# Performance work log

Measured on AMD Instinct MI355X. Metric: run time of the kernel, lower is better.

Reference implementation:

```python
import jax, jax.numpy as jnp
import numpy as np

N = 100000   # nodes
E = 1600000  # edges (avg degree 16)
F = 64       # conv_out_dim (= in_channels here)
EDGE_DIM = 16
B = 64       # graphs in batch
DEG = np.array([0, 1000, 2000, 4000, 8000, 16000, 24000, 20000, 12000, 6000, 3000, 2000, 1000, 500, 300, 200, 100], dtype=np.float64)
AVG_LOG = float((np.log(np.arange(len(DEG)) + 1.0) * DEG).sum() / DEG.sum())  # avg_deg['log']

def setup_inputs() -> dict:
    key = jax.random.key(0)
    ks = jax.random.split(key, 16)
    def w(k, shape, fan_in):
        return (jax.random.normal(k, shape, jnp.float32) / np.sqrt(fan_in)).astype(jnp.float32)
    return {
        "x": jax.random.normal(ks[0], (N, F), jnp.float32),
        "edge_attr": jax.random.normal(ks[1], (E, EDGE_DIM), jnp.float32),
        "edge_index": jax.random.randint(ks[2], (2, E), 0, N, jnp.int32),
        "batch": jnp.sort(jax.random.randint(ks[3], (N,), 0, B, jnp.int32)),
        # pre_mlp: Linear(F, F//2) -> ReLU -> Linear(F//2, F)
        "W1": w(ks[4], (F, F // 2), F), "b1": jnp.zeros((F // 2,), jnp.float32),
        "W2": w(ks[5], (F // 2, F), F // 2), "b2": jnp.zeros((F,), jnp.float32),
        # CEALConv (PNA-style) params
        "We": w(ks[6], (EDGE_DIM, F), EDGE_DIM), "be": jnp.zeros((F,), jnp.float32),   # edge encoder
        "Wp": w(ks[7], (3 * F, F), 3 * F), "bp": jnp.zeros((F,), jnp.float32),          # pre_nn
        "Wo": w(ks[8], (13 * F, F), 13 * F), "bo": jnp.zeros((F,), jnp.float32),        # post_nn ((4 agg * 3 scalers + 1) * F)
        "Wl": w(ks[9], (F, F), F), "bl": jnp.zeros((F,), jnp.float32),                  # final lin
        # BatchNorm affine
        "gamma": jnp.ones((F,), jnp.float32), "beta": jnp.zeros((F,), jnp.float32),
        # post_mlp: Linear(F, 100) -> ReLU -> Linear(100, 1)
        "Wm1": w(ks[10], (F, 100), F), "bm1": jnp.zeros((100,), jnp.float32),
        "Wm2": w(ks[11], (100, 1), 100), "bm2": jnp.zeros((1,), jnp.float32),
    }

def reference(x, edge_attr, edge_index, batch, W1, b1, W2, b2, We, be, Wp, bp, Wo, bo, Wl, bl, gamma, beta, Wm1, bm1, Wm2, bm2):
    src, dst = edge_index[0], edge_index[1]
    # pre-MLP on node features
    x = jax.nn.relu(x @ W1 + b1) @ W2 + b2                                  # [N, F]
    # message: pre_nn(cat[x_i, x_j, edge_encoder(edge_attr)]) -- split Wp to avoid concat
    e = edge_attr @ We + be                                                 # [E, F]
    h = x[dst] @ Wp[:F] + x[src] @ Wp[F:2 * F] + e @ Wp[2 * F:] + bp        # [E, F]
    # multi-aggregator scatter (mean, min, max, std) at destination nodes
    cnt = jax.ops.segment_sum(jnp.ones((E,), h.dtype), dst, N)              # in-degree [N]
    d = jnp.maximum(cnt, 1.0)[:, None]
    mean = jax.ops.segment_sum(h, dst, N) / d
    mean2 = jax.ops.segment_sum(h * h, dst, N) / d
    std = jnp.sqrt(jax.nn.relu(mean2 - mean * mean) + 1e-5)
    has = (cnt > 0)[:, None]
    mn = jnp.where(has, jax.ops.segment_min(h, dst, N), 0.0)
    mx = jnp.where(has, jax.ops.segment_max(h, dst, N), 0.0)
    agg = jnp.concatenate([mean, mn, mx, std], axis=-1)                     # [N, 4F]
    # degree scalers: identity, amplification, attenuation
    amp = jnp.log(d + 1.0) / AVG_LOG
    scaled = jnp.concatenate([agg, agg * amp, agg / amp], axis=-1)          # [N, 12F]
    # post_nn(cat[x, scaled]) then final linear
    out = jnp.concatenate([x, scaled], axis=-1) @ Wo + bo                   # [N, F]
    out = out @ Wl + bl
    # BatchNorm (batch statistics) + ReLU
    mu = out.mean(axis=0)
    var = out.var(axis=0)
    out = (out - mu) * jax.lax.rsqrt(var + 1e-5) * gamma + beta
    out = jax.nn.relu(out)
    # global_add_pool over graphs, then post-MLP head
    pooled = jax.ops.segment_sum(out, batch, B)                             # [B, F]
    return jax.nn.relu(pooled @ Wm1 + bm1) @ Wm2 + bm2                      # [B, 1]
```

## Files before the change

### kernel.cpp

```cpp
#include <hip/hip_runtime.h>
#include <hip/hip_bf16.h>
#include <math.h>

#define NN 100000
#define NE 1600000
#define FF 64
#define NB 64
#define NSCAN_BLOCKS 391

__device__ __constant__ float AVG_LOG_F = 1.9595436f;

typedef short short8 __attribute__((ext_vector_type(8)));
typedef float f32x4 __attribute__((ext_vector_type(4)));

__device__ __forceinline__ void atomAddF(float* p, float v) {
    __hip_atomic_fetch_add(p, v, __ATOMIC_RELAXED, __HIP_MEMORY_SCOPE_AGENT);
}
__device__ __forceinline__ float bf2f(short v) {
    return __uint_as_float(((unsigned)(unsigned short)v) << 16);
}
__device__ __forceinline__ unsigned packbf2(float a, float b) {
    unsigned ua = (unsigned)(unsigned short)__bfloat16_as_short(__float2bfloat16(a));
    unsigned ub = (unsigned)(unsigned short)__bfloat16_as_short(__float2bfloat16(b));
    return ua | (ub << 16);
}
__device__ __forceinline__ unsigned lds_pair(const unsigned short* p) {
    unsigned u;
    __builtin_memcpy(&u, p, 4);
    return u;
}
__device__ __forceinline__ float dot2bf(unsigned a, unsigned b, float c) {
    float d;
    asm("v_dot2_f32_bf16 %0, %1, %2, %3" : "=v"(d) : "v"(a), "v"(b), "v"(c));
    return d;
}

__global__ void fold_weights(const float* __restrict__ Wo, const float* __restrict__ Wl,
                             const float* __restrict__ bo, const float* __restrict__ bl,
                             const float* __restrict__ We, const float* __restrict__ Wp,
                             const float* __restrict__ bp, const float* __restrict__ be,
                             __hip_bfloat16* __restrict__ Wtb,
                             unsigned* __restrict__ Wepp,
                             float* __restrict__ bpF, float* __restrict__ boF) {
    int t = blockIdx.x * blockDim.x + threadIdx.x;
    if (t < 832 * 64) {
        int k = t >> 6, f = t & 63;
        float acc = 0.f;
        for (int j = 0; j < 64; j++) acc += Wo[k * 64 + j] * Wl[j * 64 + f];
        Wtb[f * 832 + k] = __float2bfloat16(acc);
    } else if (t < 832 * 64 + 512) {
        int u = t - 832 * 64; int k2 = u >> 6, f = u & 63;
        float a0 = 0.f, a1 = 0.f;
        for (int j = 0; j < 64; j++) {
            float wp = Wp[(128 + j) * 64 + f];
            a0 += We[(2 * k2) * 64 + j] * wp;
            a1 += We[(2 * k2 + 1) * 64 + j] * wp;
        }
        Wepp[k2 * 64 + f] = packbf2(a0, a1);
    } else if (t < 832 * 64 + 512 + 64) {
        int f = t - (832 * 64 + 512);
        float acc = bl[f];
        for (int j = 0; j < 64; j++) acc += bo[j] * Wl[j * 64 + f];
        boF[f] = acc;
    } else if (t < 832 * 64 + 512 + 128) {
        int f = t - (832 * 64 + 512 + 64);
        float acc = bp[f];
        for (int j = 0; j < 64; j++) acc += be[j] * Wp[(128 + j) * 64 + f];
        bpF[f] = acc;
    }
}

__global__ __launch_bounds__(256) void node_pre(const float* __restrict__ x,
                                                const float* __restrict__ W1, const float* __restrict__ b1,
                                                const float* __restrict__ W2, const float* __restrict__ b2,
                                                const float* __restrict__ Wp,
                                                float* __restrict__ x2, float* __restrict__ A,
                                                __hip_bfloat16* __restrict__ Bnb) {
    __shared__ unsigned short xs[4][64], ts[4][32], x2s[4][64];
    int tid = threadIdx.x;
    int w = tid >> 6, f = tid & 63;
    int fm = f & 31;

    unsigned w1p[32], w2p[16], wp0p[32], wp1p[32];
    #pragma unroll
    for (int k2 = 0; k2 < 32; ++k2)
        w1p[k2] = packbf2(W1[(2 * k2) * 32 + fm], W1[(2 * k2 + 1) * 32 + fm]);
    #pragma unroll
    for (int k2 = 0; k2 < 16; ++k2)
        w2p[k2] = packbf2(W2[(2 * k2) * 64 + f], W2[(2 * k2 + 1) * 64 + f]);
    #pragma unroll
    for (int k2 = 0; k2 < 32; ++k2) {
        wp0p[k2] = packbf2(Wp[(2 * k2) * 64 + f], Wp[(2 * k2 + 1) * 64 + f]);
        wp1p[k2] = packbf2(Wp[4096 + (2 * k2) * 64 + f], Wp[4096 + (2 * k2 + 1) * 64 + f]);
    }
    float b1f = b1[fm], b2f = b2[f];

    int wid = blockIdx.x * 4 + w;
    int nw = gridDim.x * 4;
    for (int v = wid; v < NN; v += nw) {
        float xv = x[(size_t)v * 64 + f];
        xs[w][f] = (unsigned short)__bfloat16_as_short(__float2bfloat16(xv));
        float t = b1f;
        #pragma unroll
        for (int k2 = 0; k2 < 32; ++k2) t = dot2bf(lds_pair(&xs[w][2 * k2]), w1p[k2], t);
        t = fmaxf(t, 0.f);
        if (f < 32) ts[w][f] = (unsigned short)__bfloat16_as_short(__float2bfloat16(t));
        float acc2 = b2f;
        #pragma unroll
        for (int k2 = 0; k2 < 16; ++k2) acc2 = dot2bf(lds_pair(&ts[w][2 * k2]), w2p[k2], acc2);
        x2[(size_t)v * 64 + f] = acc2;
        x2s[w][f] = (unsigned short)__bfloat16_as_short(__float2bfloat16(acc2));
        float aa = 0.f, bb = 0.f;
        #pragma unroll
        for (int k2 = 0; k2 < 32; ++k2) {
            unsigned xq = lds_pair(&x2s[w][2 * k2]);
            aa = dot2bf(xq, wp0p[k2], aa);
            bb = dot2bf(xq, wp1p[k2], bb);
        }
        A[(size_t)v * 64 + f] = aa;
        Bnb[(size_t)v * 64 + f] = __float2bfloat16(bb);
    }
}

__global__ void hist_kernel(const int* __restrict__ ei, unsigned* __restrict__ cnt_i) {
    int t = blockIdx.x * blockDim.x + threadIdx.x;
    if (t < NE) atomicAdd(&cnt_i[ei[NE + t]], 1u);
}

__global__ void scan_blocksum(const unsigned* __restrict__ cnt_i, unsigned* __restrict__ bsum) {
    __shared__ unsigned red[256];
    int t = blockIdx.x * 256 + threadIdx.x;
    unsigned c = (t < NN) ? cnt_i[t] : 0u;
    red[threadIdx.x] = c; __syncthreads();
    for (int s = 128; s > 0; s >>= 1) {
        if (threadIdx.x < s) red[threadIdx.x] += red[threadIdx.x + s];
        __syncthreads();
    }
    if (threadIdx.x == 0) bsum[blockIdx.x] = red[0];
}

__global__ void scan_top(const unsigned* __restrict__ bsum, unsigned* __restrict__ boff,
                         unsigned* __restrict__ start) {
    __shared__ unsigned sh[512];
    int t = threadIdx.x;
    unsigned v = (t < NSCAN_BLOCKS) ? bsum[t] : 0u;
    sh[t] = v; __syncthreads();
    for (int d = 1; d < 512; d <<= 1) {
        unsigned add = (t >= d) ? sh[t - d] : 0u;
        __syncthreads();
        sh[t] += add;
        __syncthreads();
    }
    if (t < NSCAN_BLOCKS) boff[t] = sh[t] - v;
    if (t == 0) start[NN] = NE;
}

__global__ void scan_final(const unsigned* __restrict__ cnt_i, const unsigned* __restrict__ boff,
                           unsigned* __restrict__ start) {
    __shared__ unsigned sh[256];
    int b = blockIdx.x, t = threadIdx.x;
    int v = b * 256 + t;
    unsigned c = (v < NN) ? cnt_i[v] : 0u;
    sh[t] = c; __syncthreads();
    for (int d = 1; d < 256; d <<= 1) {
        unsigned add = (t >= d) ? sh[t - d] : 0u;
        __syncthreads();
        sh[t] += add;
        __syncthreads();
    }
    if (v < NN) start[v] = boff[b] + sh[t] - c;
}

__global__ void scatter_kernel(const int* __restrict__ ei, const float* __restrict__ ea,
                               const unsigned* __restrict__ start,
                               unsigned* __restrict__ cnt_i,
                               __hip_bfloat16* __restrict__ eab, int* __restrict__ src_s) {
    int t = blockIdx.x * blockDim.x + threadIdx.x;
    if (t == 0) {
        src_s[NE] = 0;
        short8 z = {0, 0, 0, 0, 0, 0, 0, 0};
        short8* p = (short8*)(eab + (size_t)NE * 16);
        p[0] = z; p[1] = z;
    }
    if (t < NE) {
        int d = ei[NE + t];
        unsigned old = atomicSub(&cnt_i[d], 1u);
        unsigned pos = start[d] + old - 1u;
        src_s[pos] = ei[t];
        const float4* s4 = (const float4*)(ea + (size_t)t * 16);
        float4 a = s4[0], b = s4[1], c = s4[2], e = s4[3];
        short8 o0, o1;
        o0[0] = (short)__bfloat16_as_short(__float2bfloat16(a.x));
        o0[1] = (short)__bfloat16_as_short(__float2bfloat16(a.y));
        o0[2] = (short)__bfloat16_as_short(__float2bfloat16(a.z));
        o0[3] = (short)__bfloat16_as_short(__float2bfloat16(a.w));
        o0[4] = (short)__bfloat16_as_short(__float2bfloat16(b.x));
        o0[5] = (short)__bfloat16_as_short(__float2bfloat16(b.y));
        o0[6] = (short)__bfloat16_as_short(__float2bfloat16(b.z));
        o0[7] = (short)__bfloat16_as_short(__float2bfloat16(b.w));
        o1[0] = (short)__bfloat16_as_short(__float2bfloat16(c.x));
        o1[1] = (short)__bfloat16_as_short(__float2bfloat16(c.y));
        o1[2] = (short)__bfloat16_as_short(__float2bfloat16(c.z));
        o1[3] = (short)__bfloat16_as_short(__float2bfloat16(c.w));
        o1[4] = (short)__bfloat16_as_short(__float2bfloat16(e.x));
        o1[5] = (short)__bfloat16_as_short(__float2bfloat16(e.y));
        o1[6] = (short)__bfloat16_as_short(__float2bfloat16(e.z));
        o1[7] = (short)__bfloat16_as_short(__float2bfloat16(e.w));
        short8* dst8 = (short8*)(eab + (size_t)pos * 16);
        dst8[0] = o0; dst8[1] = o1;
    }
}

__global__ __launch_bounds__(256) void deg_localhist(const unsigned* __restrict__ start,
                                                     unsigned* __restrict__ bh,
                                                     unsigned* __restrict__ rank_g) {
    __shared__ unsigned short keys[256];
    int t0 = threadIdx.x, b = blockIdx.x;
    int t = b * 256 + t0;
    unsigned d = 0xFFFFu;
    if (t < NN) {
        d = start[t + 1] - start[t];
        if (d > 255u) d = 255u;
    }
    keys[t0] = (unsigned short)d;
    __syncthreads();
    unsigned cnt = 0;
    #pragma unroll 8
    for (int i = 0; i < 256; ++i) cnt += (keys[i] == (unsigned short)t0) ? 1u : 0u;
    bh[t0 * NSCAN_BLOCKS + b] = cnt;
    if (t < NN) {
        unsigned r = 0;
        for (int i = 0; i < t0; ++i) r += (keys[i] == (unsigned short)d) ? 1u : 0u;
        rank_g[t] = r;
    }
}

__global__ __launch_bounds__(256) void deg_colscan(const unsigned* __restrict__ bh,
                                                   unsigned* __restrict__ bhoff) {
    __shared__ unsigned sh[256];
    int bin = threadIdx.x;
    unsigned s = 0;
    for (int b = 0; b < NSCAN_BLOCKS; ++b) s += bh[bin * NSCAN_BLOCKS + b];
    sh[bin] = s;
    __syncthreads();
    for (int d = 1; d < 256; d <<= 1) {
        unsigned add = (bin >= d) ? sh[bin - d] : 0u;
        __syncthreads();
        sh[bin] += add;
        __syncthreads();
    }
    unsigned run = sh[bin] - s;
    for (int b = 0; b < NSCAN_BLOCKS; ++b) {
        unsigned c = bh[bin * NSCAN_BLOCKS + b];
        bhoff[bin * NSCAN_BLOCKS + b] = run;
        run += c;
    }
}

__global__ __launch_bounds__(256) void deg_place(const unsigned* __restrict__ start,
                                                 const unsigned* __restrict__ bhoff,
                                                 const unsigned* __restrict__ rank_g,
                                                 int* __restrict__ perm) {
    int t0 = threadIdx.x, b = blockIdx.x;
    int t = b * 256 + t0;
    if (t < NN) {
        unsigned d = start[t + 1] - start[t];
        if (d > 255u) d = 255u;
        perm[bhoff[d * NSCAN_BLOCKS + b] + rank_g[t]] = t;
    }
}

__global__ __launch_bounds__(256) void agg_post_kernel(const __hip_bfloat16* __restrict__ eab,
                                                       const int* __restrict__ src_s,
                                                       const unsigned* __restrict__ start,
                                                       const int* __restrict__ perm,
                                                       const float* __restrict__ A,
                                                       const unsigned short* __restrict__ Bnb,
                                                       const float* __restrict__ x2,
                                                       const unsigned* __restrict__ Wepp, const float* __restrict__ bpF,
                                                       const __hip_bfloat16* __restrict__ Wtb,
                                                       const float* __restrict__ boF,
                                                       float* __restrict__ out_pre,
                                                       float* __restrict__ bnsum, float* __restrict__ bnsum2) {
    __shared__ __hip_bfloat16 As[16 * 840];
    __shared__ int pvs[16];
    int tid = threadIdx.x;
    int w = __builtin_amdgcn_readfirstlane(tid >> 6);
    int f = tid & 63;
    int base = blockIdx.x * 16;

    unsigned wcolp[8];
    #pragma unroll
    for (int k = 0; k < 8; k++) wcolp[k] = Wepp[k * 64 + f];
    float bpf = bpF[f];

    int vv[4]; unsigned s0[4]; int len[4], lim[4]; float av[4];
    float sA[4] = {0.f, 0.f, 0.f, 0.f}, s2A[4] = {0.f, 0.f, 0.f, 0.f};
    float mnA[4], mxA[4];
    int maxlen = 0;
    #pragma unroll
    for (int g = 0; g < 4; ++g) {
        int v = __builtin_amdgcn_readfirstlane(perm[base + g * 4 + w]);
        vv[g] = v;
        if (f == 0) pvs[g * 4 + w] = v;
        unsigned a = start[v], b = start[v + 1];
        s0[g] = a; len[g] = (int)(b - a);
        lim[g] = len[g] > 0 ? len[g] - 1 : 0;
        maxlen = max(maxlen, len[g]);
        av[g] = A[(size_t)v * 64 + f] + bpf;
        mnA[g] = INFINITY; mxA[g] = -INFINITY;
    }

    for (int j = 0; j < maxlen; ++j) {
        #pragma unroll
        for (int g = 0; g < 4; ++g) {
            unsigned idx = s0[g] + (unsigned)min(j, lim[g]);
            const unsigned* e32 = (const unsigned*)(eab + (size_t)idx * 16);
            int src = src_s[idx];
            const unsigned short* brow = Bnb + ((size_t)src << 6);
            float h = av[g];
            #pragma unroll
            for (int k = 0; k < 8; k++) h = dot2bf(e32[k], wcolp[k], h);
            h += bf2f((short)brow[f]);
            bool valid = j < len[g];
            float hm = valid ? h : 0.f;
            sA[g] += hm; s2A[g] += hm * hm;
            mnA[g] = fminf(mnA[g], h);
            mxA[g] = fmaxf(mxA[g], h);
        }
    }

    #pragma unroll
    for (int g = 0; g < 4; ++g) {
        int n = g * 4 + w;
        int v = vv[g];
        float c = (float)len[g];
        float d = fmaxf(c, 1.f);
        float inv = 1.f / d;
        float mean = sA[g] * inv, mean2 = s2A[g] * inv;
        float sd = sqrtf(fmaxf(mean2 - mean * mean, 0.f) + 1e-5f);
        bool has = len[g] > 0;
        float mn = has ? mnA[g] : 0.f;
        float mx = has ? mxA[g] : 0.f;
        float l = __logf(d + 1.f);
        float amp = l * (1.0f / 1.9595436f);
        float iamp = 1.9595436f / l;
        __hip_bfloat16* row = &As[n * 840];
        row[f]        = __float2bfloat16(x2[(size_t)v * 64 + f]);
        row[64 + f]   = __float2bfloat16(mean);
        row[128 + f]  = __float2bfloat16(mn);
        row[192 + f]  = __float2bfloat16(mx);
        row[256 + f]  = __float2bfloat16(sd);
        row[320 + f]  = __float2bfloat16(mean * amp);
        row[384 + f]  = __float2bfloat16(mn * amp);
        row[448 + f]  = __float2bfloat16(mx * amp);
        row[512 + f]  = __float2bfloat16(sd * amp);
        row[576 + f]  = __float2bfloat16(mean * iamp);
        row[640 + f]  = __float2bfloat16(mn * iamp);
        row[704 + f]  = __float2bfloat16(mx * iamp);
        row[768 + f]  = __float2bfloat16(sd * iamp);
    }
    __syncthreads();

    int m = f & 15, q = f >> 4;
    int fbase = w * 16;
    f32x4 acc = {0.f, 0.f, 0.f, 0.f};
    const __hip_bfloat16* arow = &As[m * 840 + q * 8];
    const __hip_bfloat16* brow = &Wtb[(size_t)(fbase + m) * 832 + q * 8];
    #pragma unroll
    for (int s = 0; s < 26; ++s) {
        short8 af = *(const short8*)(arow + s * 32);
        short8 bf = *(const short8*)(brow + s * 32);
        acc = __builtin_amdgcn_mfma_f32_16x16x32_bf16(af, bf, acc, 0, 0, 0);
    }

    float bof = boF[fbase + m];
    float p1 = 0.f, p2 = 0.f;
    #pragma unroll
    for (int r = 0; r < 4; ++r) {
        float vvv = acc[r] + bof;
        int vn = pvs[q * 4 + r];
        out_pre[(size_t)vn * 64 + fbase + m] = vvv;
        p1 += vvv; p2 += vvv * vvv;
    }
    p1 += __shfl_xor(p1, 16); p2 += __shfl_xor(p2, 16);
    p1 += __shfl_xor(p1, 32); p2 += __shfl_xor(p2, 32);
    if (f < 16) {
        atomAddF(&bnsum[fbase + f], p1);
        atomAddF(&bnsum2[fbase + f], p2);
    }
}

__global__ __launch_bounds__(256) void bn_pool(const float* __restrict__ out_pre, const int* __restrict__ batch,
                                               const float* __restrict__ bnsum, const float* __restrict__ bnsum2,
                                               const float* __restrict__ gamma, const float* __restrict__ beta,
                                               float* __restrict__ pooled) {
    __shared__ float red[256];
    int tid = threadIdx.x, f = tid & 63, q = tid >> 6;
    int base = blockIdx.x * 64;
    float mu = bnsum[f] * (1.0f / NN);
    float var = bnsum2[f] * (1.0f / NN) - mu * mu;
    float sc = gamma[f] * rsqrtf(var + 1e-5f);
    float sh = beta[f] - mu * sc;
    int b_first = batch[base < NN ? base : NN - 1];
    int last = base + 63; if (last >= NN) last = NN - 1;
    int b_last = batch[last];
    if (b_first == b_last) {
        float local = 0.f;
        for (int g = 0; g < 16; ++g) {
            int v = base + g * 4 + q;
            if (v < NN) local += fmaxf(out_pre[(size_t)v * 64 + f] * sc + sh, 0.f);
        }
        red[tid] = local;
        __syncthreads();
        if (tid < 64) atomAddF(&pooled[b_first * 64 + f], red[f] + red[f + 64] + red[f + 128] + red[f + 192]);
    } else {
        for (int g = 0; g < 16; ++g) {
            int v = base + g * 4 + q;
            if (v < NN) {
                float val = fmaxf(out_pre[(size_t)v * 64 + f] * sc + sh, 0.f);
                atomAddF(&pooled[batch[v] * 64 + f], val);
            }
        }
    }
}

__global__ void head_kernel(const float* __restrict__ pooled,
                            const float* __restrict__ Wm1, const float* __restrict__ bm1,
                            const float* __restrict__ Wm2, const float* __restrict__ bm2,
                            float* __restrict__ out) {
    __shared__ float ts[64][104];
    int tid = threadIdx.x;
    for (int t = tid; t < 64 * 100; t += 256) {
        int b = t / 100, j = t % 100;
        float acc = bm1[j];
        for (int k = 0; k < 64; k++) acc += pooled[b * 64 + k] * Wm1[k * 100 + j];
        ts[b][j] = fmaxf(acc, 0.f);
    }
    __syncthreads();
    if (tid < 64) {
        float acc = bm2[0];
        for (int j = 0; j < 100; j++) acc += ts[tid][j] * Wm2[j];
        out[tid] = acc;
    }
}

extern "C" void kernel_launch(void* const* d_in, const int* in_sizes, int n_in,
                              void* d_out, int out_size, void* d_ws, size_t ws_size,
                              hipStream_t stream) {
    const float* x    = (const float*)d_in[0];
    const float* ea   = (const float*)d_in[1];
    const int*   ei   = (const int*)d_in[2];
    const int*   batch= (const int*)d_in[3];
    const float* W1   = (const float*)d_in[4];
    const float* b1   = (const float*)d_in[5];
    const float* W2   = (const float*)d_in[6];
    const float* b2   = (const float*)d_in[7];
    const float* We   = (const float*)d_in[8];
    const float* be   = (const float*)d_in[9];
    const float* Wp   = (const float*)d_in[10];
    const float* bp   = (const float*)d_in[11];
    const float* Wo   = (const float*)d_in[12];
    const float* bo   = (const float*)d_in[13];
    const float* Wl   = (const float*)d_in[14];
    const float* bl   = (const float*)d_in[15];
    const float* gamma= (const float*)d_in[16];
    const float* beta = (const float*)d_in[17];
    const float* Wm1  = (const float*)d_in[18];
    const float* bm1  = (const float*)d_in[19];
    const float* Wm2  = (const float*)d_in[20];
    const float* bm2  = (const float*)d_in[21];

    float* ws = (float*)d_ws;
    constexpr size_t NF = (size_t)NN * 64;
    const size_t o_x2     = 0;
    const size_t o_B      = NF;
    const size_t o_A      = 2 * NF;
    const size_t o_outpre = 3 * NF;
    const size_t o_start  = 4 * NF;
    const size_t o_cnt_i  = o_start + 100016;
    const size_t o_bsum   = o_cnt_i + 100000;
    const size_t o_boff   = o_bsum + 512;
    const size_t o_perm   = o_boff + 512;
    const size_t o_eab    = o_perm + 100000;
    const size_t o_srcs   = o_eab + 12800016;
    const size_t o_Wtb    = o_srcs + 1600016;
    const size_t o_Wepp   = o_Wtb + 26624;
    const size_t o_bpF    = o_Wepp + 512;
    const size_t o_boF    = o_bpF + 64;
    const size_t o_bnscale= o_boF + 64;
    const size_t o_bnshift= o_bnscale + 64;
    const size_t o_pooled = o_bnshift + 64;
    const size_t o_bnsum  = o_pooled + 64 * 64;
    const size_t o_bnsum2 = o_bnsum + 64;

    unsigned* bh     = (unsigned*)(ws + o_cnt_i);
    unsigned* bhoff  = (unsigned*)(ws + o_outpre);
    unsigned* rank_g = (unsigned*)(ws + o_outpre + 100096);

    hipMemsetAsync(ws + o_cnt_i, 0, 100000 * sizeof(unsigned), stream);
    hipMemsetAsync(ws + o_pooled, 0, (64 * 64 + 128) * sizeof(float), stream);

    fold_weights<<<213, 256, 0, stream>>>(Wo, Wl, bo, bl, We, Wp, bp, be,
                                          (__hip_bfloat16*)(ws + o_Wtb), (unsigned*)(ws + o_Wepp),
                                          ws + o_bpF, ws + o_boF);
    node_pre<<<768, 256, 0, stream>>>(x, W1, b1, W2, b2, Wp,
                                      ws + o_x2, ws + o_A, (__hip_bfloat16*)(ws + o_B));
    hist_kernel<<<6250, 256, 0, stream>>>(ei, (unsigned*)(ws + o_cnt_i));
    scan_blocksum<<<NSCAN_BLOCKS, 256, 0, stream>>>((unsigned*)(ws + o_cnt_i), (unsigned*)(ws + o_bsum));
    scan_top<<<1, 512, 0, stream>>>((unsigned*)(ws + o_bsum), (unsigned*)(ws + o_boff),
                                    (unsigned*)(ws + o_start));
    scan_final<<<NSCAN_BLOCKS, 256, 0, stream>>>((unsigned*)(ws + o_cnt_i), (unsigned*)(ws + o_boff),
                                                 (unsigned*)(ws + o_start));
    scatter_kernel<<<6250, 256, 0, stream>>>(ei, ea, (const unsigned*)(ws + o_start),
                                             (unsigned*)(ws + o_cnt_i),
                                             (__hip_bfloat16*)(ws + o_eab), (int*)(ws + o_srcs));
    deg_localhist<<<NSCAN_BLOCKS, 256, 0, stream>>>((const unsigned*)(ws + o_start), bh, rank_g);
    deg_colscan<<<1, 256, 0, stream>>>(bh, bhoff);
    deg_place<<<NSCAN_BLOCKS, 256, 0, stream>>>((const unsigned*)(ws + o_start), bhoff, rank_g,
                                                (int*)(ws + o_perm));
    agg_post_kernel<<<6250, 256, 0, stream>>>((const __hip_bfloat16*)(ws + o_eab),
                                              (const int*)(ws + o_srcs),
                                              (const unsigned*)(ws + o_start),
                                              (const int*)(ws + o_perm),
                                              ws + o_A, (const unsigned short*)(ws + o_B), ws + o_x2,
                                              (const unsigned*)(ws + o_Wepp), ws + o_bpF,
                                              (const __hip_bfloat16*)(ws + o_Wtb), ws + o_boF,
                                              ws + o_outpre, ws + o_bnsum, ws + o_bnsum2);
    bn_pool<<<1563, 256, 0, stream>>>(ws + o_outpre, batch,
                                      ws + o_bnsum, ws + o_bnsum2, gamma, beta, ws + o_pooled);
    head_kernel<<<1, 256, 0, stream>>>(ws + o_pooled, Wm1, bm1, Wm2, bm2, (float*)d_out);
}
```

Baseline: 733.8 us.

## Fuse histogram into node_pre, merge degree sort into scan, software-pipeline aggregation loop

The edge in-degree histogram moves into node_pre as a grid-stride loop, which removes one kernel launch. The degree-bucket local histogram and rank computation are folded into the final scan kernel, and degree placement now runs before scatter using cnt_i, which scatter still needs. The agg loop processes two edges per iteration and prefetches src indices and B rows two iterations ahead to hide gather latency. This costs more registers and could lower occupancy.

```diff
diff --git a/kernel.cpp b/kernel.cpp
--- a/kernel.cpp
+++ b/kernel.cpp
@@ -74,6 +74,7 @@
                                                 const float* __restrict__ W1, const float* __restrict__ b1,
                                                 const float* __restrict__ W2, const float* __restrict__ b2,
                                                 const float* __restrict__ Wp,
+                                                const int* __restrict__ ei, unsigned* __restrict__ cnt_i,
                                                 float* __restrict__ x2, float* __restrict__ A,
                                                 __hip_bfloat16* __restrict__ Bnb) {
     __shared__ unsigned short xs[4][64], ts[4][32], x2s[4][64];
@@ -81,6 +82,10 @@
     int w = tid >> 6, f = tid & 63;
     int fm = f & 31;
 
+    int nthreads = gridDim.x * 256;
+    for (int e = blockIdx.x * 256 + tid; e < NE; e += nthreads)
+        atomicAdd(&cnt_i[ei[NE + e]], 1u);
+
     unsigned w1p[32], w2p[16], wp0p[32], wp1p[32];
     #pragma unroll
     for (int k2 = 0; k2 < 32; ++k2)
@@ -120,11 +125,6 @@
         A[(size_t)v * 64 + f] = aa;
         Bnb[(size_t)v * 64 + f] = __float2bfloat16(bb);
     }
-}
-
-__global__ void hist_kernel(const int* __restrict__ ei, unsigned* __restrict__ cnt_i) {
-    int t = blockIdx.x * blockDim.x + threadIdx.x;
-    if (t < NE) atomicAdd(&cnt_i[ei[NE + t]], 1u);
 }
 
 __global__ void scan_blocksum(const unsigned* __restrict__ cnt_i, unsigned* __restrict__ bsum) {
@@ -155,20 +155,72 @@
     if (t == 0) start[NN] = NE;
 }
 
-__global__ void scan_final(const unsigned* __restrict__ cnt_i, const unsigned* __restrict__ boff,
-                           unsigned* __restrict__ start) {
+__global__ __launch_bounds__(256) void scan_final_deg(const unsigned* __restrict__ cnt_i,
+                                                      const unsigned* __restrict__ boff,
+                                                      unsigned* __restrict__ start,
+                                                      unsigned* __restrict__ bh,
+                                                      unsigned* __restrict__ rank_g) {
     __shared__ unsigned sh[256];
+    __shared__ unsigned short keys[256];
     int b = blockIdx.x, t = threadIdx.x;
     int v = b * 256 + t;
     unsigned c = (v < NN) ? cnt_i[v] : 0u;
-    sh[t] = c; __syncthreads();
+    sh[t] = c;
+    unsigned d = 0xFFFFu;
+    if (v < NN) d = (c > 255u) ? 255u : c;
+    keys[t] = (unsigned short)d;
+    __syncthreads();
+    for (int dd = 1; dd < 256; dd <<= 1) {
+        unsigned add = (t >= dd) ? sh[t - dd] : 0u;
+        __syncthreads();
+        sh[t] += add;
+        __syncthreads();
+    }
+    if (v < NN) start[v] = boff[b] + sh[t] - c;
+    unsigned cnt = 0;
+    #pragma unroll 8
+    for (int i = 0; i < 256; ++i) cnt += (keys[i] == (unsigned short)t) ? 1u : 0u;
+    bh[t * NSCAN_BLOCKS + b] = cnt;
+    if (v < NN) {
+        unsigned r = 0;
+        for (int i = 0; i < t; ++i) r += (keys[i] == (unsigned short)d) ? 1u : 0u;
+        rank_g[v] = r;
+    }
+}
+
+__global__ __launch_bounds__(256) void deg_colscan(const unsigned* __restrict__ bh,
+                                                   unsigned* __restrict__ bhoff) {
+    __shared__ unsigned sh[256];
+    int bin = threadIdx.x;
+    unsigned s = 0;
+    for (int b = 0; b < NSCAN_BLOCKS; ++b) s += bh[bin * NSCAN_BLOCKS + b];
+    sh[bin] = s;
+    __syncthreads();
     for (int d = 1; d < 256; d <<= 1) {
-        unsigned add = (t >= d) ? sh[t - d] : 0u;
-        __syncthreads();
-        sh[t] += add;
-        __syncthreads();
-    }
-    if (v < NN) start[v] = boff[b] + sh[t] - c;
+        unsigned add = (bin >= d) ? sh[bin - d] : 0u;
+        __syncthreads();
+        sh[bin] += add;
+        __syncthreads();
+    }
+    unsigned run = sh[bin] - s;
+    for (int b = 0; b < NSCAN_BLOCKS; ++b) {
+        unsigned c = bh[bin * NSCAN_BLOCKS + b];
+        bhoff[bin * NSCAN_BLOCKS + b] = run;
+        run += c;
+    }
+}
+
+__global__ __launch_bounds__(256) void deg_place(const unsigned* __restrict__ cnt_i,
+                                                 const unsigned* __restrict__ bhoff,
+                                                 const unsigned* __restrict__ rank_g,
+                                                 int* __restrict__ perm) {
+    int t0 = threadIdx.x, b = blockIdx.x;
+    int t = b * 256 + t0;
+    if (t < NN) {
+        unsigned d = cnt_i[t];
+        if (d > 255u) d = 255u;
+        perm[bhoff[d * NSCAN_BLOCKS + b] + rank_g[t]] = t;
+    }
 }
 
 __global__ void scatter_kernel(const int* __restrict__ ei, const float* __restrict__ ea,
@@ -211,65 +263,6 @@
     }
 }
 
-__global__ __launch_bounds__(256) void deg_localhist(const unsigned* __restrict__ start,
-                                                     unsigned* __restrict__ bh,
-                                                     unsigned* __restrict__ rank_g) {
-    __shared__ unsigned short keys[256];
-    int t0 = threadIdx.x, b = blockIdx.x;
-    int t = b * 256 + t0;
-    unsigned d = 0xFFFFu;
-    if (t < NN) {
-        d = start[t + 1] - start[t];
-        if (d > 255u) d = 255u;
-    }
-    keys[t0] = (unsigned short)d;
-    __syncthreads();
-    unsigned cnt = 0;
-    #pragma unroll 8
-    for (int i = 0; i < 256; ++i) cnt += (keys[i] == (unsigned short)t0) ? 1u : 0u;
-    bh[t0 * NSCAN_BLOCKS + b] = cnt;
-    if (t < NN) {
-        unsigned r = 0;
-        for (int i = 0; i < t0; ++i) r += (keys[i] == (unsigned short)d) ? 1u : 0u;
-        rank_g[t] = r;
-    }
-}
-
-__global__ __launch_bounds__(256) void deg_colscan(const unsigned* __restrict__ bh,
-                                                   unsigned* __restrict__ bhoff) {
-    __shared__ unsigned sh[256];
-    int bin = threadIdx.x;
-    unsigned s = 0;
-    for (int b = 0; b < NSCAN_BLOCKS; ++b) s += bh[bin * NSCAN_BLOCKS + b];
-    sh[bin] = s;
-    __syncthreads();
-    for (int d = 1; d < 256; d <<= 1) {
-        unsigned add = (bin >= d) ? sh[bin - d] : 0u;
-        __syncthreads();
-        sh[bin] += add;
-        __syncthreads();
-    }
-    unsigned run = sh[bin] - s;
-    for (int b = 0; b < NSCAN_BLOCKS; ++b) {
-        unsigned c = bh[bin * NSCAN_BLOCKS + b];
-        bhoff[bin * NSCAN_BLOCKS + b] = run;
-        run += c;
-    }
-}
-
-__global__ __launch_bounds__(256) void deg_place(const unsigned* __restrict__ start,
-                                                 const unsigned* __restrict__ bhoff,
-                                                 const unsigned* __restrict__ rank_g,
-                                                 int* __restrict__ perm) {
-    int t0 = threadIdx.x, b = blockIdx.x;
-    int t = b * 256 + t0;
-    if (t < NN) {
-        unsigned d = start[t + 1] - start[t];
-        if (d > 255u) d = 255u;
-        perm[bhoff[d * NSCAN_BLOCKS + b] + rank_g[t]] = t;
-    }
-}
-
 __global__ __launch_bounds__(256) void agg_post_kernel(const __hip_bfloat16* __restrict__ eab,
                                                        const int* __restrict__ src_s,
                                                        const unsigned* __restrict__ start,
@@ -311,22 +304,59 @@
         mnA[g] = INFINITY; mxA[g] = -INFINITY;
     }
 
-    for (int j = 0; j < maxlen; ++j) {
+    int sP0[4], sP1[4];
+    float bnC0[4], bnC1[4];
+    #pragma unroll
+    for (int g = 0; g < 4; ++g) {
+        int a0 = src_s[s0[g]];
+        int a1 = src_s[s0[g] + (unsigned)min(1, lim[g])];
+        bnC0[g] = bf2f((short)Bnb[((size_t)a0 << 6) + f]);
+        bnC1[g] = bf2f((short)Bnb[((size_t)a1 << 6) + f]);
+        sP0[g] = src_s[s0[g] + (unsigned)min(2, lim[g])];
+        sP1[g] = src_s[s0[g] + (unsigned)min(3, lim[g])];
+    }
+
+    for (int j = 0; j < maxlen; j += 2) {
+        int sN0[4], sN1[4];
+        float bnN0[4], bnN1[4];
+        unsigned e0[4][8], e1[4][8];
         #pragma unroll
         for (int g = 0; g < 4; ++g) {
-            unsigned idx = s0[g] + (unsigned)min(j, lim[g]);
-            const unsigned* e32 = (const unsigned*)(eab + (size_t)idx * 16);
-            int src = src_s[idx];
-            const unsigned short* brow = Bnb + ((size_t)src << 6);
-            float h = av[g];
+            sN0[g] = src_s[s0[g] + (unsigned)min(j + 4, lim[g])];
+            sN1[g] = src_s[s0[g] + (unsigned)min(j + 5, lim[g])];
+            bnN0[g] = bf2f((short)Bnb[((size_t)sP0[g] << 6) + f]);
+            bnN1[g] = bf2f((short)Bnb[((size_t)sP1[g] << 6) + f]);
+            const unsigned* p0 = (const unsigned*)(eab + (size_t)(s0[g] + (unsigned)min(j, lim[g])) * 16);
+            const unsigned* p1 = (const unsigned*)(eab + (size_t)(s0[g] + (unsigned)min(j + 1, lim[g])) * 16);
             #pragma unroll
-            for (int k = 0; k < 8; k++) h = dot2bf(e32[k], wcolp[k], h);
-            h += bf2f((short)brow[f]);
+            for (int k = 0; k < 8; ++k) { e0[g][k] = p0[k]; e1[g][k] = p1[k]; }
+        }
+        #pragma unroll
+        for (int g = 0; g < 4; ++g) {
+            float h = av[g] + bnC0[g];
+            #pragma unroll
+            for (int k = 0; k < 8; k++) h = dot2bf(e0[g][k], wcolp[k], h);
             bool valid = j < len[g];
             float hm = valid ? h : 0.f;
             sA[g] += hm; s2A[g] += hm * hm;
             mnA[g] = fminf(mnA[g], h);
             mxA[g] = fmaxf(mxA[g], h);
+        }
+        #pragma unroll
+        for (int g = 0; g < 4; ++g) {
+            float h = av[g] + bnC1[g];
+            #pragma unroll
+            for (int k = 0; k < 8; k++) h = dot2bf(e1[g][k], wcolp[k], h);
+            bool valid = (j + 1) < len[g];
+            float hm = valid ? h : 0.f;
+            sA[g] += hm; s2A[g] += hm * hm;
+            mnA[g] = fminf(mnA[g], h);
+            mxA[g] = fmaxf(mxA[g], h);
+        }
+        #pragma unroll
+        for (int g = 0; g < 4; ++g) {
+            bnC0[g] = bnN0[g]; bnC1[g] = bnN1[g];
+            sP0[g] = sN0[g];   sP1[g] = sN1[g];
         }
     }
 
@@ -488,15 +518,13 @@
     const size_t o_Wepp   = o_Wtb + 26624;
     const size_t o_bpF    = o_Wepp + 512;
     const size_t o_boF    = o_bpF + 64;
-    const size_t o_bnscale= o_boF + 64;
-    const size_t o_bnshift= o_bnscale + 64;
-    const size_t o_pooled = o_bnshift + 64;
+    const size_t o_pooled = o_boF + 64;
     const size_t o_bnsum  = o_pooled + 64 * 64;
     const size_t o_bnsum2 = o_bnsum + 64;
 
-    unsigned* bh     = (unsigned*)(ws + o_cnt_i);
     unsigned* bhoff  = (unsigned*)(ws + o_outpre);
     unsigned* rank_g = (unsigned*)(ws + o_outpre + 100096);
+    unsigned* bh     = (unsigned*)(ws + o_outpre + 200096);
 
     hipMemsetAsync(ws + o_cnt_i, 0, 100000 * sizeof(unsigned), stream);
     hipMemsetAsync(ws + o_pooled, 0, (64 * 64 + 128) * sizeof(float), stream);
@@ -505,20 +533,19 @@
                                           (__hip_bfloat16*)(ws + o_Wtb), (unsigned*)(ws + o_Wepp),
                                           ws + o_bpF, ws + o_boF);
     node_pre<<<768, 256, 0, stream>>>(x, W1, b1, W2, b2, Wp,
+                                      ei, (unsigned*)(ws + o_cnt_i),
                                       ws + o_x2, ws + o_A, (__hip_bfloat16*)(ws + o_B));
-    hist_kernel<<<6250, 256, 0, stream>>>(ei, (unsigned*)(ws + o_cnt_i));
     scan_blocksum<<<NSCAN_BLOCKS, 256, 0, stream>>>((unsigned*)(ws + o_cnt_i), (unsigned*)(ws + o_bsum));
     scan_top<<<1, 512, 0, stream>>>((unsigned*)(ws + o_bsum), (unsigned*)(ws + o_boff),
                                     (unsigned*)(ws + o_start));
-    scan_final<<<NSCAN_BLOCKS, 256, 0, stream>>>((unsigned*)(ws + o_cnt_i), (unsigned*)(ws + o_boff),
-                                                 (unsigned*)(ws + o_start));
+    scan_final_deg<<<NSCAN_BLOCKS, 256, 0, stream>>>((unsigned*)(ws + o_cnt_i), (unsigned*)(ws + o_boff),
+                                                     (unsigned*)(ws + o_start), bh, rank_g);
+    deg_colscan<<<1, 256, 0, stream>>>(bh, bhoff);
+    deg_place<<<NSCAN_BLOCKS, 256, 0, stream>>>((const unsigned*)(ws + o_cnt_i), bhoff, rank_g,
+                                                (int*)(ws + o_perm));
     scatter_kernel<<<6250, 256, 0, stream>>>(ei, ea, (const unsigned*)(ws + o_start),
                                              (unsigned*)(ws + o_cnt_i),
                                              (__hip_bfloat16*)(ws + o_eab), (int*)(ws + o_srcs));
-    deg_localhist<<<NSCAN_BLOCKS, 256, 0, stream>>>((const unsigned*)(ws + o_start), bh, rank_g);
-    deg_colscan<<<1, 256, 0, stream>>>(bh, bhoff);
-    deg_place<<<NSCAN_BLOCKS, 256, 0, stream>>>((const unsigned*)(ws + o_start), bhoff, rank_g,
-                                                (int*)(ws + o_perm));
     agg_post_kernel<<<6250, 256, 0, stream>>>((const __hip_bfloat16*)(ws + o_eab),
                                               (const int*)(ws + o_srcs),
                                               (const unsigned*)(ws + o_start),
```

Result: faster. 688.5 us (-6.2%).
